# Performance work log

Measured on AMD Instinct MI355X. Metric: run time of the kernel, lower is better.

Reference implementation:

```python
import jax, jax.numpy as jnp
import numpy as np

B, OBS, H, N = 16384, 512, 1024, 9

def setup_inputs() -> dict:
    key = jax.random.key(0)
    ks = jax.random.split(key, 12)
    s = 0.02
    return {
        "obs": jax.random.normal(ks[0], (B, OBS), jnp.float32),
        "agent_positions": jax.random.normal(ks[1], (B, N, 3), jnp.float32),
        "W1": jax.random.normal(ks[2], (OBS, H), jnp.float32) * s,
        "b1": jnp.zeros((H,), jnp.float32),
        "W2": jax.random.normal(ks[3], (H, H), jnp.float32) * s,
        "b2": jnp.zeros((H,), jnp.float32),
        "Wc1": jax.random.normal(ks[4], (H, H // 2), jnp.float32) * s,
        "bc1": jnp.zeros((H // 2,), jnp.float32),
        "Wc2": jax.random.normal(ks[5], (H // 2, 1), jnp.float32) * s,
        "bc2": jnp.zeros((1,), jnp.float32),
        "Wt1": jax.random.normal(ks[6], (H, H // 2), jnp.float32) * s,
        "bt1": jnp.zeros((H // 2,), jnp.float32),
        "Wt2": jax.random.normal(ks[7], (H // 2, 1), jnp.float32) * s,
        "bt2": jnp.zeros((1,), jnp.float32),
        "Wk1": jax.random.normal(ks[8], (2 * H, H), jnp.float32) * s,
        "bk1": jnp.zeros((H,), jnp.float32),
        "Wk2": jax.random.normal(ks[9], (H, 1), jnp.float32) * s,
        "bk2": jnp.zeros((1,), jnp.float32),
    }


def reference(obs, agent_positions, W1, b1, W2, b2, Wc1, bc1, Wc2, bc2,
              Wt1, bt1, Wt2, bt2, Wk1, bk1, Wk2, bk2):
    # global features: Linear->ReLU->Linear->ReLU
    g = jax.nn.relu(obs @ W1 + b1)
    g = jax.nn.relu(g @ W2 + b2)  # [B, H]

    # Each per-agent head is applied to the SAME g in the original loop,
    # so one pass + broadcast is mathematically identical.
    cov = jax.nn.sigmoid(jax.nn.relu(g @ Wc1 + bc1) @ Wc2 + bc2)  # [B,1]
    trk = jax.nn.sigmoid(jax.nn.relu(g @ Wt1 + bt1) @ Wt2 + bt2)  # [B,1]
    coop_in = jnp.concatenate([g, g], axis=-1)                    # [B,2H]
    coop = jax.nn.sigmoid(jax.nn.relu(coop_in @ Wk1 + bk1) @ Wk2 + bk2)  # [B,1]
    # mean over 8 identical cooperation scores == the score itself

    coverage = jnp.broadcast_to(cov, (cov.shape[0], N))      # [B, N]
    tracking = jnp.broadcast_to(trk, (trk.shape[0], N))      # [B, N]
    cooperation = jnp.broadcast_to(coop, (coop.shape[0], N)) # [B, N]
    return (coverage, tracking, cooperation)
```

## Files before the change

kernel.cpp:

```cpp
#include <hip/hip_runtime.h>
#include <hip/hip_bf16.h>

#define B_ROWS 16384
#define OBS_D  512
#define H_D    1024
#define N_AG   9

typedef __attribute__((ext_vector_type(8))) short short8;
typedef __attribute__((ext_vector_type(4))) float floatx4;

__device__ __forceinline__ unsigned short f_to_bf_raw(float f) {
  union { float f; unsigned u; } c; c.f = f;
  unsigned u = c.u;
  u = u + 0x7FFF + ((u >> 16) & 1);
  return (unsigned short)(u >> 16);
}

__global__ __launch_bounds__(256) void prep_all(
    const float* __restrict__ obs,
    const float* __restrict__ W1, const float* __restrict__ W2,
    const float* __restrict__ Wc1, const float* __restrict__ Wt1,
    const float* __restrict__ Wk1,
    const float* __restrict__ bc1, const float* __restrict__ bt1,
    const float* __restrict__ bk1,
    const float* __restrict__ Wc2, const float* __restrict__ Wt2,
    const float* __restrict__ Wk2,
    unsigned short* __restrict__ obs_bf,
    unsigned short* __restrict__ W1T, unsigned short* __restrict__ W2T,
    unsigned short* __restrict__ WH,
    float* __restrict__ bias2048, float* __restrict__ w2cat) {
  __shared__ float t[32][33];
  const int bx  = blockIdx.x;
  const int tid = threadIdx.x;

  if (bx < 4096) {
    int i = (bx * 256 + tid) * 8;
    float4 a = *(const float4*)(obs + i);
    float4 b = *(const float4*)(obs + i + 4);
    short8 o;
    o[0] = (short)f_to_bf_raw(a.x); o[1] = (short)f_to_bf_raw(a.y);
    o[2] = (short)f_to_bf_raw(a.z); o[3] = (short)f_to_bf_raw(a.w);
    o[4] = (short)f_to_bf_raw(b.x); o[5] = (short)f_to_bf_raw(b.y);
    o[6] = (short)f_to_bf_raw(b.z); o[7] = (short)f_to_bf_raw(b.w);
    *(short8*)(obs_bf + i) = o;
    return;
  }

  const int tx = tid & 31;
  const int ty = tid >> 5;

  if (bx < 4608) {
    const int tt = bx - 4096;
    const int k0 = (tt & 15) * 32;
    const int n0 = (tt >> 4) * 32;
#pragma unroll
    for (int i = ty; i < 32; i += 8)
      t[i][tx] = W1[(size_t)(k0 + i) * 1024 + n0 + tx];
    __syncthreads();
#pragma unroll
    for (int i = ty; i < 32; i += 8)
      W1T[(size_t)(n0 + i) * 512 + k0 + tx] = f_to_bf_raw(t[tx][i]);
    return;
  }

  if (bx < 5632) {
    const int tt = bx - 4608;
    const int k0 = (tt & 31) * 32;
    const int n0 = (tt >> 5) * 32;
#pragma unroll
    for (int i = ty; i < 32; i += 8)
      t[i][tx] = W2[(size_t)(k0 + i) * 1024 + n0 + tx];
    __syncthreads();
#pragma unroll
    for (int i = ty; i < 32; i += 8)
      W2T[(size_t)(n0 + i) * 1024 + k0 + tx] = f_to_bf_raw(t[tx][i]);
    return;
  }

  if (bx < 7680) {
    const int tt = bx - 5632;
    const int k0 = (tt & 31) * 32;
    const int n0 = (tt >> 5) * 32;
#pragma unroll
    for (int i = ty; i < 32; i += 8) {
      const int n = n0 + tx;
      float v;
      if (n0 < 512)
        v = Wc1[(size_t)(k0 + i) * 512 + n];
      else if (n0 < 1024)
        v = Wt1[(size_t)(k0 + i) * 512 + (n - 512)];
      else
        v = Wk1[(size_t)(k0 + i) * 1024 + (n - 1024)]
          + Wk1[(size_t)(k0 + i + 1024) * 1024 + (n - 1024)];
      t[i][tx] = v;
    }
    __syncthreads();
#pragma unroll
    for (int i = ty; i < 32; i += 8)
      WH[(size_t)(n0 + i) * 1024 + k0 + tx] = f_to_bf_raw(t[tx][i]);
    return;
  }

  {
    int n = (bx - 7680) * 256 + tid;
    float b, w;
    if (n < 512)       { b = bc1[n];        w = Wc2[n]; }
    else if (n < 1024) { b = bt1[n - 512];  w = Wt2[n - 512]; }
    else               { b = bk1[n - 1024]; w = Wk2[n - 1024]; }
    bias2048[n] = b;
    w2cat[n] = w;
  }
}

#define GLD_LDS(gp, lp)                                                        \
  __builtin_amdgcn_global_load_lds(                                            \
      (const __attribute__((address_space(1))) void*)(gp),                     \
      (__attribute__((address_space(3))) void*)(lp), 16, 0, 0)

#define GEMM_CORE_V6(ACC_DECL)                                                 \
  __shared__ __align__(16) unsigned short As[2][128 * 32];                     \
  __shared__ __align__(16) unsigned short Bs[2][128 * 32];                     \
  const int tid  = threadIdx.x;                                                \
  const int lane = tid & 63;                                                   \
  const int wave = tid >> 6;                                                   \
  const int m0 = blockIdx.x * 128;                                             \
  const int n0 = blockIdx.y * 128;                                             \
  const int wm = (wave & 1) * 64;                                              \
  const int wn = (wave >> 1) * 64;                                             \
  const int fr = lane & 15;                                                    \
  const int fq = lane >> 4;                                                    \
  ACC_DECL;                                                                    \
  const size_t rowb = (size_t)K * 2;                                           \
  const int srow   = lane >> 2;                                                \
  const int schunk = (lane & 3) ^ ((srow >> 1) & 3);                           \
  const char* gA0 = (const char*)A + (size_t)(m0 + wave * 32 + srow) * rowb    \
                    + schunk * 16;                                             \
  const char* gA1 = gA0 + 16 * rowb;                                           \
  const char* gB0 = (const char*)Bt + (size_t)(n0 + wave * 32 + srow) * rowb   \
                    + schunk * 16;                                             \
  const char* gB1 = gB0 + 16 * rowb;                                           \
  char* lA = (char*)&As[0][0] + (wave * 32) * 64 + lane * 16;                  \
  char* lB = (char*)&Bs[0][0] + (wave * 32) * 64 + lane * 16;                  \
  const int fswz = (fr >> 1) & 3;                                              \
  const int fsA = (wm + fr) * 64 + ((fq ^ fswz) * 16);                         \
  const int fsB = (wn + fr) * 64 + ((fq ^ fswz) * 16);                         \
  constexpr int nIter = K >> 5;                                                \
           \
  GLD_LDS(gA0, lA);        GLD_LDS(gA1, lA + 1024);                            \
  GLD_LDS(gB0, lB);        GLD_LDS(gB1, lB + 1024);                            \
  gA0 += 64; gA1 += 64; gB0 += 64; gB1 += 64;                                  \
  __syncthreads();                                                             \
  GLD_LDS(gA0, lA + 8192); GLD_LDS(gA1, lA + 9216);                            \
  GLD_LDS(gB0, lB + 8192); GLD_LDS(gB1, lB + 9216);                            \
  gA0 += 64; gA1 += 64; gB0 += 64; gB1 += 64;                                  \
  short8 Fa[2][4], Fb[2][4];                                                   \
  _Pragma("unroll")                                                            \
  for (int mi = 0; mi < 4; ++mi)                                               \
    Fa[0][mi] = *(const short8*)((const char*)&As[0][0] + fsA + mi * 1024);    \
  _Pragma("unroll")                                                            \
  for (int ni = 0; ni < 4; ++ni)                                               \
    Fb[0][ni] = *(const short8*)((const char*)&Bs[0][0] + fsB + ni * 1024);    \
  _Pragma("unroll")                                                            \
  for (int k = 0; k < nIter; ++k) {        \
    const int cur = k & 1;                     \
    __syncthreads();                                                           \
    if (k + 2 < nIter) {                                                       \
      char* dA = lA + cur * 8192;                                              \
      char* dB = lB + cur * 8192;                                              \
      GLD_LDS(gA0, dA); GLD_LDS(gA1, dA + 1024);                               \
      GLD_LDS(gB0, dB); GLD_LDS(gB1, dB + 1024);                               \
      gA0 += 64; gA1 += 64; gB0 += 64; gB1 += 64;                              \
    }                                                                          \
    if (k + 1 < nIter) {                                                       \
      const char* bAs = (const char*)&As[0][0] + (cur ^ 1) * 8192;             \
      const char* bBs = (const char*)&Bs[0][0] + (cur ^ 1) * 8192;             \
      _Pragma("unroll")                                                        \
      for (int mi = 0; mi < 4; ++mi)                                           \
        Fa[cur ^ 1][mi] = *(const short8*)(bAs + fsA + mi * 1024);             \
      _Pragma("unroll")                                                        \
      for (int ni = 0; ni < 4; ++ni)                                           \
        Fb[cur ^ 1][ni] = *(const short8*)(bBs + fsB + ni * 1024);             \
    }                                                                          \
    _Pragma("unroll")                                                          \
    for (int mi = 0; mi < 4; ++mi)                                             \
      _Pragma("unroll")                                                        \
      for (int ni = 0; ni < 4; ++ni)                                           \
        acc[mi][ni] = __builtin_amdgcn_mfma_f32_16x16x32_bf16(                 \
            Fa[cur][mi], Fb[cur][ni], acc[mi][ni], 0, 0, 0);                   \
  }

#define ACC_INIT                                                               \
  floatx4 acc[4][4];                                                           \
  _Pragma("unroll")                                                            \
  for (int i = 0; i < 4; ++i)                                                  \
    _Pragma("unroll")                                                          \
    for (int j = 0; j < 4; ++j) acc[i][j] = (floatx4){0.f, 0.f, 0.f, 0.f}

template <int K>
__global__ __launch_bounds__(256, 3) void gemm_bias_relu(
    const unsigned short* __restrict__ A,
    const unsigned short* __restrict__ Bt,
    const float* __restrict__ bias,
    unsigned short* __restrict__ C,
    int M, int N) {
  GEMM_CORE_V6(ACC_INIT)

#pragma unroll
  for (int ni = 0; ni < 4; ++ni) {
    const int gn = n0 + wn + ni * 16 + fr;
    const float bv = bias[gn];
#pragma unroll
    for (int mi = 0; mi < 4; ++mi) {
#pragma unroll
      for (int r = 0; r < 4; ++r) {
        const int gm = m0 + wm + mi * 16 + fq * 4 + r;
        float v = acc[mi][ni][r] + bv;
        v = v > 0.f ? v : 0.f;
        C[(size_t)gm * N + gn] = f_to_bf_raw(v);
      }
    }
  }
}

template <int K>
__global__ __launch_bounds__(256, 3) void gemm_heads_fused(
    const unsigned short* __restrict__ A,
    const unsigned short* __restrict__ Bt,
    const float* __restrict__ bias,
    const float* __restrict__ w2,
    float* __restrict__ part,
    int M, int N) {
  GEMM_CORE_V6(ACC_INIT)

  const int j = blockIdx.y * 2 + (wave >> 1);
  float w2v[4], bv[4];
#pragma unroll
  for (int ni = 0; ni < 4; ++ni) {
    const int gn = n0 + wn + ni * 16 + fr;
    w2v[ni] = w2[gn];
    bv[ni]  = bias[gn];
  }
#pragma unroll
  for (int mi = 0; mi < 4; ++mi) {
#pragma unroll
    for (int r = 0; r < 4; ++r) {
      float p = 0.f;
#pragma unroll
      for (int ni = 0; ni < 4; ++ni) {
        float v = acc[mi][ni][r] + bv[ni];
        v = v > 0.f ? v : 0.f;
        p += v * w2v[ni];
      }
      p += __shfl_xor(p, 1);
      p += __shfl_xor(p, 2);
      p += __shfl_xor(p, 4);
      p += __shfl_xor(p, 8);
      if (fr == 0) {
        const int gm = m0 + wm + mi * 16 + fq * 4 + r;
        part[(size_t)j * B_ROWS + gm] = p;
      }
    }
  }
}

__global__ __launch_bounds__(256) void final_out(
    const float* __restrict__ part,
    const float* __restrict__ bc2, const float* __restrict__ bt2,
    const float* __restrict__ bk2, float* __restrict__ out) {
  const int row = blockIdx.x * 256 + threadIdx.x;
  float sc = 0.f, st = 0.f, sk = 0.f;
#pragma unroll
  for (int j = 0; j < 8; ++j)  sc += part[(size_t)j * B_ROWS + row];
#pragma unroll
  for (int j = 8; j < 16; ++j) st += part[(size_t)j * B_ROWS + row];
#pragma unroll
  for (int j = 16; j < 32; ++j) sk += part[(size_t)j * B_ROWS + row];
  const float cv = 1.f / (1.f + expf(-(sc + bc2[0])));
  const float tv = 1.f / (1.f + expf(-(st + bt2[0])));
  const float kv = 1.f / (1.f + expf(-(sk + bk2[0])));
  float* o0 = out + (size_t)row * N_AG;
  float* o1 = out + (size_t)(B_ROWS + row) * N_AG;
  float* o2 = out + (size_t)(2 * B_ROWS + row) * N_AG;
#pragma unroll
  for (int a = 0; a < N_AG; ++a) { o0[a] = cv; o1[a] = tv; o2[a] = kv; }
}

extern "C" void kernel_launch(void* const* d_in, const int* in_sizes, int n_in,
                              void* d_out, int out_size, void* d_ws, size_t ws_size,
                              hipStream_t stream) {
  const float* obs = (const float*)d_in[0];
  const float* W1  = (const float*)d_in[2];
  const float* b1  = (const float*)d_in[3];
  const float* W2  = (const float*)d_in[4];
  const float* b2  = (const float*)d_in[5];
  const float* Wc1 = (const float*)d_in[6];
  const float* bc1 = (const float*)d_in[7];
  const float* Wc2 = (const float*)d_in[8];
  const float* bc2 = (const float*)d_in[9];
  const float* Wt1 = (const float*)d_in[10];
  const float* bt1 = (const float*)d_in[11];
  const float* Wt2 = (const float*)d_in[12];
  const float* bt2 = (const float*)d_in[13];
  const float* Wk1 = (const float*)d_in[14];
  const float* bk1 = (const float*)d_in[15];
  const float* Wk2 = (const float*)d_in[16];
  const float* bk2 = (const float*)d_in[17];
  float* out = (float*)d_out;

  char* ws = (char*)d_ws;
  unsigned short* obs_bf  = (unsigned short*)(ws + 0);
  float*          PART    = (float*)(ws + 0);
  unsigned short* W1T     = (unsigned short*)(ws + 16777216);
  unsigned short* W2T     = (unsigned short*)(ws + 17825792);
  unsigned short* WH      = (unsigned short*)(ws + 19922944);
  float*          bias2048= (float*)(ws + 24117248);
  float*          w2cat   = (float*)(ws + 24125440);
  unsigned short* G1      = (unsigned short*)(ws + 24330240);
  unsigned short* G       = (unsigned short*)(ws + 57884672);

  prep_all<<<7688, 256, 0, stream>>>(obs, W1, W2, Wc1, Wt1, Wk1,
                                     bc1, bt1, bk1, Wc2, Wt2, Wk2,
                                     obs_bf, W1T, W2T, WH, bias2048, w2cat);

  gemm_bias_relu<512><<<dim3(128, 8), 256, 0, stream>>>(obs_bf, W1T, b1, G1, B_ROWS, 1024);
  gemm_bias_relu<1024><<<dim3(128, 8), 256, 0, stream>>>(G1, W2T, b2, G, B_ROWS, 1024);

  gemm_heads_fused<1024><<<dim3(128, 16), 256, 0, stream>>>(G, WH, bias2048, w2cat, PART,
                                                            B_ROWS, 2048);

  final_out<<<B_ROWS / 256, 256, 0, stream>>>(PART, bc2, bt2, bk2, out);
}
```

Measured before the change: 294.4 us.

## Pre-pack weights in MFMA fragment order and load B fragments directly from global

The prep kernel now writes the bf16 weight matrices in a layout that matches the MFMA B-fragment order per 16x32 tile. The GEMM kernels drop the B shared-memory staging and have each lane read its short8 fragment straight from global memory, double-buffered in registers. This removes LDS traffic, LDS space and global-to-LDS copies for B. The cost is that the four waves sharing a 64-column slice now read the same B data separately through the cache, and global load latency is exposed inside the k loop.

```diff
diff --git a/kernel.cpp b/kernel.cpp
--- a/kernel.cpp
+++ b/kernel.cpp
@@ -14,6 +14,12 @@
   unsigned u = c.u;
   u = u + 0x7FFF + ((u >> 16) & 1);
   return (unsigned short)(u >> 16);
+}
+
+__device__ __forceinline__ size_t frag_off(int n, int k, int KT) {
+  const int ft = (n >> 4) * KT + (k >> 5);
+  const int ln = (n & 15) | (((k >> 3) & 3) << 4);
+  return ((size_t)ft * 64 + ln) * 8 + (k & 7);
 }
 
 __global__ __launch_bounds__(256) void prep_all(
@@ -26,8 +32,8 @@
     const float* __restrict__ Wc2, const float* __restrict__ Wt2,
     const float* __restrict__ Wk2,
     unsigned short* __restrict__ obs_bf,
-    unsigned short* __restrict__ W1T, unsigned short* __restrict__ W2T,
-    unsigned short* __restrict__ WH,
+    unsigned short* __restrict__ W1f, unsigned short* __restrict__ W2f,
+    unsigned short* __restrict__ WHf,
     float* __restrict__ bias2048, float* __restrict__ w2cat) {
   __shared__ float t[32][33];
   const int bx  = blockIdx.x;
@@ -59,7 +65,7 @@
     __syncthreads();
 #pragma unroll
     for (int i = ty; i < 32; i += 8)
-      W1T[(size_t)(n0 + i) * 512 + k0 + tx] = f_to_bf_raw(t[tx][i]);
+      W1f[frag_off(n0 + i, k0 + tx, 16)] = f_to_bf_raw(t[tx][i]);
     return;
   }
 
@@ -73,7 +79,7 @@
     __syncthreads();
 #pragma unroll
     for (int i = ty; i < 32; i += 8)
-      W2T[(size_t)(n0 + i) * 1024 + k0 + tx] = f_to_bf_raw(t[tx][i]);
+      W2f[frag_off(n0 + i, k0 + tx, 32)] = f_to_bf_raw(t[tx][i]);
     return;
   }
 
@@ -97,7 +103,7 @@
     __syncthreads();
 #pragma unroll
     for (int i = ty; i < 32; i += 8)
-      WH[(size_t)(n0 + i) * 1024 + k0 + tx] = f_to_bf_raw(t[tx][i]);
+      WHf[frag_off(n0 + i, k0 + tx, 32)] = f_to_bf_raw(t[tx][i]);
     return;
   }
 
@@ -117,9 +123,8 @@
       (const __attribute__((address_space(1))) void*)(gp),                     \
       (__attribute__((address_space(3))) void*)(lp), 16, 0, 0)
 
-#define GEMM_CORE_V6(ACC_DECL)                                                 \
-  __shared__ __align__(16) unsigned short As[2][128 * 32];                     \
-  __shared__ __align__(16) unsigned short Bs[2][128 * 32];                     \
+#define GEMM_CORE_V7(ACC_DECL)                                                 \
+  __shared__ __align__(16) unsigned short As[2][128 * 32];          \
   const int tid  = threadIdx.x;                                                \
   const int lane = tid & 63;                                                   \
   const int wave = tid >> 6;                                                   \
@@ -130,56 +135,50 @@
   const int fr = lane & 15;                                                    \
   const int fq = lane >> 4;                                                    \
   ACC_DECL;                                                                    \
+  constexpr int KT = K >> 5;                                                   \
+  constexpr int nIter = KT;                                                    \
   const size_t rowb = (size_t)K * 2;                                           \
   const int srow   = lane >> 2;                                                \
   const int schunk = (lane & 3) ^ ((srow >> 1) & 3);                           \
   const char* gA0 = (const char*)A + (size_t)(m0 + wave * 32 + srow) * rowb    \
                     + schunk * 16;                                             \
   const char* gA1 = gA0 + 16 * rowb;                                           \
-  const char* gB0 = (const char*)Bt + (size_t)(n0 + wave * 32 + srow) * rowb   \
-                    + schunk * 16;                                             \
-  const char* gB1 = gB0 + 16 * rowb;                                           \
   char* lA = (char*)&As[0][0] + (wave * 32) * 64 + lane * 16;                  \
-  char* lB = (char*)&Bs[0][0] + (wave * 32) * 64 + lane * 16;                  \
+  const char* gBf = (const char*)Bf                                            \
+      + (((size_t)((n0 >> 4) + (wn >> 4)) * KT) * 64 + lane) * 16;             \
   const int fswz = (fr >> 1) & 3;                                              \
   const int fsA = (wm + fr) * 64 + ((fq ^ fswz) * 16);                         \
-  const int fsB = (wn + fr) * 64 + ((fq ^ fswz) * 16);                         \
-  constexpr int nIter = K >> 5;                                                \
-           \
-  GLD_LDS(gA0, lA);        GLD_LDS(gA1, lA + 1024);                            \
-  GLD_LDS(gB0, lB);        GLD_LDS(gB1, lB + 1024);                            \
-  gA0 += 64; gA1 += 64; gB0 += 64; gB1 += 64;                                  \
+  short8 Fa[2][4], Fb[2][4];                                                   \
+      \
+  GLD_LDS(gA0, lA); GLD_LDS(gA1, lA + 1024);                                   \
+  gA0 += 64; gA1 += 64;                                                        \
   __syncthreads();                                                             \
   GLD_LDS(gA0, lA + 8192); GLD_LDS(gA1, lA + 9216);                            \
-  GLD_LDS(gB0, lB + 8192); GLD_LDS(gB1, lB + 9216);                            \
-  gA0 += 64; gA1 += 64; gB0 += 64; gB1 += 64;                                  \
-  short8 Fa[2][4], Fb[2][4];                                                   \
+  gA0 += 64; gA1 += 64;                                                        \
+  _Pragma("unroll")                                                            \
+  for (int ni = 0; ni < 4; ++ni)                                               \
+    Fb[0][ni] = *(const short8*)(gBf + (size_t)ni * (KT * 1024));              \
   _Pragma("unroll")                                                            \
   for (int mi = 0; mi < 4; ++mi)                                               \
     Fa[0][mi] = *(const short8*)((const char*)&As[0][0] + fsA + mi * 1024);    \
-  _Pragma("unroll")                                                            \
-  for (int ni = 0; ni < 4; ++ni)                                               \
-    Fb[0][ni] = *(const short8*)((const char*)&Bs[0][0] + fsB + ni * 1024);    \
   _Pragma("unroll")                                                            \
   for (int k = 0; k < nIter; ++k) {        \
     const int cur = k & 1;                     \
     __syncthreads();                                                           \
     if (k + 2 < nIter) {                                                       \
       char* dA = lA + cur * 8192;                                              \
-      char* dB = lB + cur * 8192;                                              \
       GLD_LDS(gA0, dA); GLD_LDS(gA1, dA + 1024);                               \
-      GLD_LDS(gB0, dB); GLD_LDS(gB1, dB + 1024);                               \
-      gA0 += 64; gA1 += 64; gB0 += 64; gB1 += 64;                              \
+      gA0 += 64; gA1 += 64;                                                    \
     }                                                                          \
     if (k + 1 < nIter) {                                                       \
+      _Pragma("unroll")                                                        \
+      for (int ni = 0; ni < 4; ++ni)                                           \
+        Fb[cur ^ 1][ni] =                                                      \
+            *(const short8*)(gBf + ((size_t)ni * KT + (k + 1)) * 1024);        \
       const char* bAs = (const char*)&As[0][0] + (cur ^ 1) * 8192;             \
-      const char* bBs = (const char*)&Bs[0][0] + (cur ^ 1) * 8192;             \
       _Pragma("unroll")                                                        \
       for (int mi = 0; mi < 4; ++mi)                                           \
         Fa[cur ^ 1][mi] = *(const short8*)(bAs + fsA + mi * 1024);             \
-      _Pragma("unroll")                                                        \
-      for (int ni = 0; ni < 4; ++ni)                                           \
-        Fb[cur ^ 1][ni] = *(const short8*)(bBs + fsB + ni * 1024);             \
     }                                                                          \
     _Pragma("unroll")                                                          \
     for (int mi = 0; mi < 4; ++mi)                                             \
@@ -199,11 +198,11 @@
 template <int K>
 __global__ __launch_bounds__(256, 3) void gemm_bias_relu(
     const unsigned short* __restrict__ A,
-    const unsigned short* __restrict__ Bt,
+    const unsigned short* __restrict__ Bf,
     const float* __restrict__ bias,
     unsigned short* __restrict__ C,
     int M, int N) {
-  GEMM_CORE_V6(ACC_INIT)
+  GEMM_CORE_V7(ACC_INIT)
 
 #pragma unroll
   for (int ni = 0; ni < 4; ++ni) {
@@ -225,12 +224,12 @@
 template <int K>
 __global__ __launch_bounds__(256, 3) void gemm_heads_fused(
     const unsigned short* __restrict__ A,
-    const unsigned short* __restrict__ Bt,
+    const unsigned short* __restrict__ Bf,
     const float* __restrict__ bias,
     const float* __restrict__ w2,
     float* __restrict__ part,
     int M, int N) {
-  GEMM_CORE_V6(ACC_INIT)
+  GEMM_CORE_V7(ACC_INIT)
 
   const int j = blockIdx.y * 2 + (wave >> 1);
   float w2v[4], bv[4];
@@ -310,9 +309,9 @@
   char* ws = (char*)d_ws;
   unsigned short* obs_bf  = (unsigned short*)(ws + 0);
   float*          PART    = (float*)(ws + 0);
-  unsigned short* W1T     = (unsigned short*)(ws + 16777216);
-  unsigned short* W2T     = (unsigned short*)(ws + 17825792);
-  unsigned short* WH      = (unsigned short*)(ws + 19922944);
+  unsigned short* W1f     = (unsigned short*)(ws + 16777216);
+  unsigned short* W2f     = (unsigned short*)(ws + 17825792);
+  unsigned short* WHf     = (unsigned short*)(ws + 19922944);
   float*          bias2048= (float*)(ws + 24117248);
   float*          w2cat   = (float*)(ws + 24125440);
   unsigned short* G1      = (unsigned short*)(ws + 24330240);
@@ -320,12 +319,12 @@
 
   prep_all<<<7688, 256, 0, stream>>>(obs, W1, W2, Wc1, Wt1, Wk1,
                                      bc1, bt1, bk1, Wc2, Wt2, Wk2,
-                                     obs_bf, W1T, W2T, WH, bias2048, w2cat);
-
-  gemm_bias_relu<512><<<dim3(128, 8), 256, 0, stream>>>(obs_bf, W1T, b1, G1, B_ROWS, 1024);
-  gemm_bias_relu<1024><<<dim3(128, 8), 256, 0, stream>>>(G1, W2T, b2, G, B_ROWS, 1024);
-
-  gemm_heads_fused<1024><<<dim3(128, 16), 256, 0, stream>>>(G, WH, bias2048, w2cat, PART,
+                                     obs_bf, W1f, W2f, WHf, bias2048, w2cat);
+
+  gemm_bias_relu<512><<<dim3(128, 8), 256, 0, stream>>>(obs_bf, W1f, b1, G1, B_ROWS, 1024);
+  gemm_bias_relu<1024><<<dim3(128, 8), 256, 0, stream>>>(G1, W2f, b2, G, B_ROWS, 1024);
+
+  gemm_heads_fused<1024><<<dim3(128, 16), 256, 0, stream>>>(G, WHf, bias2048, w2cat, PART,
                                                             B_ROWS, 2048);
 
   final_out<<<B_ROWS / 256, 256, 0, stream>>>(PART, bc2, bt2, bk2, out);
```

After: 278.5 us. 5.4% less time.
